# Kernel tuning notes

Hardware: AMD Instinct MI355X
Metric: run time of the kernel (lower is better)

Reference implementation:

```python
import jax, jax.numpy as jnp
import numpy as np

DECAY = 0.5
TAU = 16
SLOPE = 0.01  # torch leaky_relu default negative_slope
EPS = 1e-12   # torch F.normalize default eps


def setup_inputs() -> dict:
    key = jax.random.key(0)
    k1, k2 = jax.random.split(key)
    B, D = 8, 8192
    x = jax.random.normal(k1, (B, D), dtype=jnp.float32)
    M = jax.random.uniform(k2, (D, D), dtype=jnp.float32)  # torch.rand(dim,dim)
    hs = jnp.zeros((1, D), dtype=jnp.float32)
    return {"x": x, "M": M, "hs": hs}


def reference(x, M, hs):
    # hs starts as zeros(1,dim) and broadcasts to (B,dim) on the first update
    hs0 = jnp.broadcast_to(hs, x.shape)

    def step(carry, _):
        hs_t, h = carry
        pre = DECAY * hs_t + h @ M                 # (B, D)
        act = jnp.where(pre >= 0, pre, SLOPE * pre)  # leaky_relu
        nrm = jnp.maximum(
            jnp.sqrt(jnp.sum(act * act, axis=1, keepdims=True)), EPS)
        hs_new = act / nrm                          # L2 normalize (dim=1)
        return (hs_new, hs_new), None

    (hs_final, _), _ = jax.lax.scan(step, (hs0, x), None, length=TAU)
    return hs_final
```

## Files before the change

kernel.cpp:

```cpp
#include <hip/hip_runtime.h>


#define DD 8192
#define BB 8
#define TAU 16
#define NT 512
#define KT 256
#define DECAYF 0.5f
#define SLOPEF 0.01f
#define EPSF 1e-12f

typedef __attribute__((ext_vector_type(8))) short short8v;
typedef __attribute__((ext_vector_type(8))) unsigned short ushort8v;
typedef __attribute__((ext_vector_type(4))) float float4v;

static __device__ __forceinline__ float b2f(unsigned short u) {
    union { unsigned int i; float f; } v; v.i = ((unsigned int)u) << 16; return v.f;
}
static __device__ __forceinline__ unsigned short f2b(float f) {
    union { float f; unsigned int i; } v; v.f = f;
    unsigned int r = v.i + 0x7FFFu + ((v.i >> 16) & 1u);
    return (unsigned short)(r >> 16);
}

__global__ __launch_bounds__(256) void pack_M_kernel(const float* __restrict__ M,
                                                     unsigned short* __restrict__ Bp) {
    const int w = threadIdx.x >> 6, l = threadIdx.x & 63;
    const unsigned int wid = blockIdx.x * 4 + w;
    const int kt = wid >> 9;
    const int nt = wid & 511;
    const int col = nt * 16 + (l & 15);
    const int k0  = kt * 32 + (l >> 4) * 8;
    const float* src = M + (size_t)k0 * DD + col;
    ushort8v o;
#pragma unroll
    for (int j = 0; j < 8; j++) o[j] = f2b(__builtin_nontemporal_load(src + (size_t)j * DD));
    *(ushort8v*)(Bp + ((size_t)nt * KT + kt) * 512 + (size_t)l * 8) = o;
}

__global__ __launch_bounds__(256) void pack_x_kernel(const float* __restrict__ x,
                                                     unsigned short* __restrict__ Ap) {
    const int w = threadIdx.x >> 6, l = threadIdx.x & 63;
    const int kt = blockIdx.x * 4 + w;
    const int row = l & 15;
    const int k0  = kt * 32 + (l >> 4) * 8;
    const float* src = x + (size_t)(row & 7) * DD + k0;
    ushort8v o;
#pragma unroll
    for (int j = 0; j < 8; j++) {
        const float v = src[j];
        const unsigned short h = f2b(v);
        o[j] = (row < 8) ? h : f2b(v - b2f(h));
    }
    *(ushort8v*)(Ap + (size_t)kt * 512 + (size_t)l * 8) = o;
}

__global__ __launch_bounds__(512) void step_kernel(const unsigned short* __restrict__ Ap_cur,
                                                   const unsigned short* __restrict__ Bp,
                                                   const float* __restrict__ act_prev,
                                                   const float* __restrict__ ss_prev,
                                                   float* __restrict__ act_new,
                                                   unsigned short* __restrict__ Ap_next,
                                                   float* __restrict__ ss_new) {
    const int tid = threadIdx.x;
    const int w = tid >> 6, l = tid & 63;
    const int bid = blockIdx.x;
    const int col0 = bid * 32;

    float4v acc0 = {0.f, 0.f, 0.f, 0.f}, acc1 = {0.f, 0.f, 0.f, 0.f};
    const unsigned short* Abase = Ap_cur + (size_t)l * 8;
    const unsigned short* B0 = Bp + ((size_t)(2 * bid)     * KT) * 512 + (size_t)l * 8;
    const unsigned short* B1 = Bp + ((size_t)(2 * bid + 1) * KT) * 512 + (size_t)l * 8;
    const int ktbase = w * 32;
#pragma unroll 4
    for (int i = 0; i < 32; i++) {
        const size_t off = (size_t)(ktbase + i) * 512;
        const short8v a  = *(const short8v*)(Abase + off);
        const short8v b0 = *(const short8v*)(B0 + off);
        const short8v b1 = *(const short8v*)(B1 + off);
        acc0 = __builtin_amdgcn_mfma_f32_16x16x32_bf16(a, b0, acc0, 0, 0, 0);
        acc1 = __builtin_amdgcn_mfma_f32_16x16x32_bf16(a, b1, acc1, 0, 0, 0);
    }

    __shared__ float red[8][16][33];
    {
        const int rbase = (l >> 4) * 4, c = l & 15;
#pragma unroll
        for (int q = 0; q < 4; q++) {
            red[w][rbase + q][c]      = acc0[q];
            red[w][rbase + q][16 + c] = acc1[q];
        }
    }
    __syncthreads();

    if (tid < 256) {
        const int r = tid >> 5, c = tid & 31;
        float s = 0.f;
#pragma unroll
        for (int u = 0; u < 8; u++) s += red[u][r][c] + red[u][r + 8][c];
        float v;
        if (ss_prev) {
            const float inv = 1.0f / fmaxf(sqrtf(ss_prev[r]), EPSF);
            v = inv * (s + DECAYF * act_prev[(size_t)r * DD + col0 + c]);
        } else {
            v = s;
        }
        const float a = (v >= 0.f) ? v : SLOPEF * v;
        act_new[(size_t)r * DD + col0 + c] = a;

        float t2 = a * a;
#pragma unroll
        for (int off = 16; off > 0; off >>= 1) t2 += __shfl_down(t2, off, 32);
        if ((tid & 31) == 0) atomicAdd(&ss_new[r], t2);

        red[0][r][c] = a;
    }
    __syncthreads();

    if (w == 0) {
        const int row = l & 15;
        const int kb  = (l >> 4) * 8;
        ushort8v o;
#pragma unroll
        for (int j = 0; j < 8; j++) {
            const float v = red[0][row & 7][kb + j];
            const unsigned short h = f2b(v);
            o[j] = (row < 8) ? h : f2b(v - b2f(h));
        }
        *(ushort8v*)(Ap_next + (size_t)bid * 512 + (size_t)l * 8) = o;
    }
}

__global__ __launch_bounds__(1024) void scale_kernel(const float* __restrict__ act,
                                                     const float* __restrict__ ss,
                                                     float* __restrict__ out) {
    const int e = blockIdx.x * 1024 + threadIdx.x;
    const float inv = 1.0f / fmaxf(sqrtf(ss[e >> 13]), EPSF);
    out[e] = act[e] * inv;
}

extern "C" void kernel_launch(void* const* d_in, const int* in_sizes, int n_in,
                              void* d_out, int out_size, void* d_ws, size_t ws_size,
                              hipStream_t stream) {
    const float* x = (const float*)d_in[0];
    const float* M = (const float*)d_in[1];

    const size_t szB = (size_t)NT * KT * 1024;
    const size_t szA = (size_t)KT * 1024;
    const size_t szF = (size_t)BB * DD * sizeof(float);
    const size_t szS = (size_t)TAU * BB * sizeof(float);

    char* p = (char*)d_ws;
    unsigned short* Bp  = (unsigned short*)p; p += szB;
    unsigned short* Ap0 = (unsigned short*)p; p += szA;
    unsigned short* Ap1 = (unsigned short*)p; p += szA;
    float* act0 = (float*)p; p += szF;
    float* act1 = (float*)p; p += szF;
    float* row_ss = (float*)p;

    hipMemsetAsync(row_ss, 0, szS, stream);
    pack_x_kernel<<<64, 256, 0, stream>>>(x, Ap0);
    pack_M_kernel<<<32768, 256, 0, stream>>>(M, Bp);

    unsigned short* Aps[2] = {Ap0, Ap1};
    float* acts[2] = {act0, act1};
    for (int t = 0; t < TAU; t++) {
        step_kernel<<<256, 512, 0, stream>>>(
            Aps[t & 1], Bp,
            acts[(t + 1) & 1],
            t ? (row_ss + (t - 1) * BB) : (const float*)nullptr,
            acts[t & 1],
            Aps[(t + 1) & 1],
            row_ss + t * BB);
    }
    scale_kernel<<<64, 1024, 0, stream>>>(acts[1], row_ss + (TAU - 1) * BB, (float*)d_out);
}
```

Measured before the change: 989.8 us.

## Split step kernel to 16 columns per block, batch loads, spread norm atomics

Each step block now computes one 16-column tile instead of two, which doubles the grid to 512 blocks so more CUs stay busy. The K loop issues eight A and B loads before the eight MFMAs to expose more memory-level parallelism. The row sum-of-squares atomics go to 8 slots per row, picked by block index, to cut contention, and readers sum those slots. In exchange each block loads the A tile for only one column tile, so A traffic doubles, and Ap_next is written by pairs of blocks, each filling half of a packed tile.

```diff
diff --git a/kernel.cpp b/kernel.cpp
--- a/kernel.cpp
+++ b/kernel.cpp
@@ -55,52 +55,54 @@
     *(ushort8v*)(Ap + (size_t)kt * 512 + (size_t)l * 8) = o;
 }
 
-__global__ __launch_bounds__(512) void step_kernel(const unsigned short* __restrict__ Ap_cur,
-                                                   const unsigned short* __restrict__ Bp,
-                                                   const float* __restrict__ act_prev,
-                                                   const float* __restrict__ ss_prev,
-                                                   float* __restrict__ act_new,
-                                                   unsigned short* __restrict__ Ap_next,
-                                                   float* __restrict__ ss_new) {
+__global__ __launch_bounds__(512, 4) void step_kernel(const unsigned short* __restrict__ Ap_cur,
+                                                      const unsigned short* __restrict__ Bp,
+                                                      const float* __restrict__ act_prev,
+                                                      const float* __restrict__ ss_prev,
+                                                      float* __restrict__ act_new,
+                                                      unsigned short* __restrict__ Ap_next,
+                                                      float* __restrict__ ss_new) {
     const int tid = threadIdx.x;
     const int w = tid >> 6, l = tid & 63;
     const int bid = blockIdx.x;
-    const int col0 = bid * 32;
+    const int col0 = bid * 16;
 
-    float4v acc0 = {0.f, 0.f, 0.f, 0.f}, acc1 = {0.f, 0.f, 0.f, 0.f};
-    const unsigned short* Abase = Ap_cur + (size_t)l * 8;
-    const unsigned short* B0 = Bp + ((size_t)(2 * bid)     * KT) * 512 + (size_t)l * 8;
-    const unsigned short* B1 = Bp + ((size_t)(2 * bid + 1) * KT) * 512 + (size_t)l * 8;
-    const int ktbase = w * 32;
-#pragma unroll 4
-    for (int i = 0; i < 32; i++) {
-        const size_t off = (size_t)(ktbase + i) * 512;
-        const short8v a  = *(const short8v*)(Abase + off);
-        const short8v b0 = *(const short8v*)(B0 + off);
-        const short8v b1 = *(const short8v*)(B1 + off);
-        acc0 = __builtin_amdgcn_mfma_f32_16x16x32_bf16(a, b0, acc0, 0, 0, 0);
-        acc1 = __builtin_amdgcn_mfma_f32_16x16x32_bf16(a, b1, acc1, 0, 0, 0);
+    float4v acc = {0.f, 0.f, 0.f, 0.f};
+    const unsigned short* Ab = Ap_cur + (size_t)(w * 32) * 512 + (size_t)l * 8;
+    const unsigned short* Bb = Bp + ((size_t)bid * KT + w * 32) * 512 + (size_t)l * 8;
+
+#pragma unroll
+    for (int i = 0; i < 32; i += 8) {
+        short8v av[8], bv[8];
+#pragma unroll
+        for (int u = 0; u < 8; u++) {
+            av[u] = *(const short8v*)(Ab + (size_t)(i + u) * 512);
+            bv[u] = *(const short8v*)(Bb + (size_t)(i + u) * 512);
+        }
+#pragma unroll
+        for (int u = 0; u < 8; u++)
+            acc = __builtin_amdgcn_mfma_f32_16x16x32_bf16(av[u], bv[u], acc, 0, 0, 0);
     }
 
-    __shared__ float red[8][16][33];
+    __shared__ float red[8][16][17];
     {
         const int rbase = (l >> 4) * 4, c = l & 15;
 #pragma unroll
-        for (int q = 0; q < 4; q++) {
-            red[w][rbase + q][c]      = acc0[q];
-            red[w][rbase + q][16 + c] = acc1[q];
-        }
+        for (int q = 0; q < 4; q++) red[w][rbase + q][c] = acc[q];
     }
     __syncthreads();
 
-    if (tid < 256) {
-        const int r = tid >> 5, c = tid & 31;
+    if (tid < 128) {
+        const int r = tid >> 4, c = tid & 15;
         float s = 0.f;
 #pragma unroll
         for (int u = 0; u < 8; u++) s += red[u][r][c] + red[u][r + 8][c];
         float v;
         if (ss_prev) {
-            const float inv = 1.0f / fmaxf(sqrtf(ss_prev[r]), EPSF);
+            float ss = 0.f;
+#pragma unroll
+            for (int u = 0; u < 8; u++) ss += ss_prev[r * 8 + u];
+            const float inv = 1.0f / fmaxf(sqrtf(ss), EPSF);
             v = inv * (s + DECAYF * act_prev[(size_t)r * DD + col0 + c]);
         } else {
             v = s;
@@ -110,16 +112,16 @@
 
         float t2 = a * a;
 #pragma unroll
-        for (int off = 16; off > 0; off >>= 1) t2 += __shfl_down(t2, off, 32);
-        if ((tid & 31) == 0) atomicAdd(&ss_new[r], t2);
+        for (int off = 8; off > 0; off >>= 1) t2 += __shfl_down(t2, off, 16);
+        if ((tid & 15) == 0) atomicAdd(&ss_new[r * 8 + (bid & 7)], t2);
 
         red[0][r][c] = a;
     }
     __syncthreads();
 
-    if (w == 0) {
+    if (w == 0 && (l >> 5) == (bid & 1)) {
         const int row = l & 15;
-        const int kb  = (l >> 4) * 8;
+        const int kb  = 8 * (l >> 4) - 16 * (bid & 1);
         ushort8v o;
 #pragma unroll
         for (int j = 0; j < 8; j++) {
@@ -127,7 +129,7 @@
             const unsigned short h = f2b(v);
             o[j] = (row < 8) ? h : f2b(v - b2f(h));
         }
-        *(ushort8v*)(Ap_next + (size_t)bid * 512 + (size_t)l * 8) = o;
+        *(ushort8v*)(Ap_next + (size_t)(bid >> 1) * 512 + (size_t)l * 8) = o;
     }
 }
 
@@ -135,7 +137,11 @@
                                                      const float* __restrict__ ss,
                                                      float* __restrict__ out) {
     const int e = blockIdx.x * 1024 + threadIdx.x;
-    const float inv = 1.0f / fmaxf(sqrtf(ss[e >> 13]), EPSF);
+    const int r = e >> 13;
+    float s = 0.f;
+#pragma unroll
+    for (int u = 0; u < 8; u++) s += ss[r * 8 + u];
+    const float inv = 1.0f / fmaxf(sqrtf(s), EPSF);
     out[e] = act[e] * inv;
 }
 
@@ -148,7 +154,7 @@
     const size_t szB = (size_t)NT * KT * 1024;
     const size_t szA = (size_t)KT * 1024;
     const size_t szF = (size_t)BB * DD * sizeof(float);
-    const size_t szS = (size_t)TAU * BB * sizeof(float);
+    const size_t szS = (size_t)TAU * BB * 8 * sizeof(float);
 
     char* p = (char*)d_ws;
     unsigned short* Bp  = (unsigned short*)p; p += szB;
@@ -165,13 +171,13 @@
     unsigned short* Aps[2] = {Ap0, Ap1};
     float* acts[2] = {act0, act1};
     for (int t = 0; t < TAU; t++) {
-        step_kernel<<<256, 512, 0, stream>>>(
+        step_kernel<<<512, 512, 0, stream>>>(
             Aps[t & 1], Bp,
             acts[(t + 1) & 1],
-            t ? (row_ss + (t - 1) * BB) : (const float*)nullptr,
+            t ? (row_ss + (t - 1) * BB * 8) : (const float*)nullptr,
             acts[t & 1],
             Aps[(t + 1) & 1],
-            row_ss + t * BB);
+            row_ss + t * BB * 8);
     }
-    scale_kernel<<<64, 1024, 0, stream>>>(acts[1], row_ss + (TAU - 1) * BB, (float*)d_out);
+    scale_kernel<<<64, 1024, 0, stream>>>(acts[1], row_ss + (TAU - 1) * BB * 8, (float*)d_out);
 }
```

Result: faster. 815.7 us (-17.6%).
